# Kernel tuning notes

Measured on AMD Instinct MI355X. Metric: run time of the kernel, lower is better.

Reference implementation:

```python
import jax, jax.numpy as jnp
import numpy as np

B, S, HID = 1, 2048, 4096
H, HKV, D = 32, 8, 128
ROT = 64  # partial_rotary_factor = 0.5
EPS = 1e-6
SCALE = D ** -0.5


def setup_inputs() -> dict:
    key = jax.random.key(0)
    ks = jax.random.split(key, 8)
    return {
        "hidden_states": jax.random.normal(ks[0], (B, S, HID), jnp.float32),
        "cos": jax.random.uniform(ks[1], (B, S, ROT), jnp.float32),
        "sin": jax.random.uniform(ks[2], (B, S, ROT), jnp.float32),
        "Wq": jax.random.normal(ks[3], (H * D, HID), jnp.float32) * 0.02,
        "Wk": jax.random.normal(ks[4], (HKV * D, HID), jnp.float32) * 0.02,
        "Wv": jax.random.normal(ks[5], (HKV * D, HID), jnp.float32) * 0.02,
        "Wo": jax.random.normal(ks[6], (H * D, HID), jnp.float32).T * 0.02,  # [HID, H*D]
        "q_norm_w": jnp.ones((D,), jnp.float32),
        "k_norm_w": jnp.ones((D,), jnp.float32),
    }


def _rmsnorm(x, w):
    var = jnp.mean(jnp.square(x), axis=-1, keepdims=True)
    return x * jax.lax.rsqrt(var + EPS) * w


def _rotate_half(x):
    x1, x2 = jnp.split(x, 2, axis=-1)
    return jnp.concatenate([-x2, x1], axis=-1)


def reference(hidden_states, cos, sin, Wq, Wk, Wv, Wo, q_norm_w, k_norm_w):
    b, s, _ = hidden_states.shape
    q = (hidden_states @ Wq.T).reshape(b, s, H, D)
    k = (hidden_states @ Wk.T).reshape(b, s, HKV, D)
    v = (hidden_states @ Wv.T).reshape(b, s, HKV, D)
    # per-head QK RMSNorm
    q = _rmsnorm(q, q_norm_w)
    k = _rmsnorm(k, k_norm_w)
    # partial RoPE on first ROT dims; cos/sin broadcast over head dim (unsqueeze_dim=2)
    cs = cos[:, :, None, :]  # [B,S,1,ROT]
    sn = sin[:, :, None, :]
    q_rot, q_pass = q[..., :ROT], q[..., ROT:]
    k_rot, k_pass = k[..., :ROT], k[..., ROT:]
    q_rot = q_rot * cs + _rotate_half(q_rot) * sn
    k_rot = k_rot * cs + _rotate_half(k_rot) * sn
    q = jnp.concatenate([q_rot, q_pass], axis=-1)
    k = jnp.concatenate([k_rot, k_pass], axis=-1)
    # GQA: expand kv heads to query heads
    rep = H // HKV
    k = jnp.repeat(k, rep, axis=2)  # [B,S,H,D]
    v = jnp.repeat(v, rep, axis=2)
    # causal SDPA, bsnd layout
    scores = jnp.einsum("bqhd,bkhd->bhqk", q, k) * SCALE
    causal = jnp.tril(jnp.ones((s, s), bool))
    scores = jnp.where(causal, scores, jnp.finfo(scores.dtype).min)
    attn = jax.nn.softmax(scores, axis=-1)
    out = jnp.einsum("bhqk,bkhd->bqhd", attn, v).reshape(b, s, H * D)
    return out @ Wo.T
```

## Files before the change

### kernel.cpp

```cpp
#include <hip/hip_runtime.h>
#include <hip/hip_bf16.h>

typedef __attribute__((ext_vector_type(8))) short bf16x8;
typedef __attribute__((ext_vector_type(4))) float f32x4;
typedef __hip_bfloat16 bf16;

#define S_LEN 2048
#define HIDDEN 4096
#define NH 32
#define NKV 8
#define DH 128
#define ROTD 64
#define QKVW 6144
#define KOFF 4096
#define VOFF 5120
#define ATT_SCALE 0.08838834764831845f
#define RMS_EPS 1e-6f
#define KPITCH 136
#define VPITCH 72

#define BAR() __builtin_amdgcn_s_barrier()
#define VMCNT(n) asm volatile("s_waitcnt vmcnt(" #n ")" ::: "memory")
#define LGKM(n)  asm volatile("s_waitcnt lgkmcnt(" #n ")" ::: "memory")

static __device__ __forceinline__ unsigned short f2bu(float f) {
    bf16 h = __float2bfloat16(f);
    return __builtin_bit_cast(unsigned short, h);
}

static __device__ __forceinline__ void load_lds_16(const bf16* g, bf16* l) {
    __builtin_amdgcn_global_load_lds((const __attribute__((address_space(1))) void*)g,
                                     (__attribute__((address_space(3))) void*)l, 16, 0, 0);
}

__global__ __launch_bounds__(256) void cast_f32_bf16(const float* __restrict__ src,
                                                     unsigned short* __restrict__ dst, int n4) {
    int i = blockIdx.x * 256 + threadIdx.x;
    if (i >= n4) return;
    float4 v = reinterpret_cast<const float4*>(src)[i];
    ushort4 o;
    o.x = f2bu(v.x); o.y = f2bu(v.y); o.z = f2bu(v.z); o.w = f2bu(v.w);
    reinterpret_cast<ushort4*>(dst)[i] = o;
}

#define LDA_SUB(bufi, half) do {                                                        \
    const bf16* _ab = &As[bufi][half][0];                                               \
    _Pragma("unroll") for (int mf = 0; mf < 4; ++mf) {                                  \
        const int _r = arow + mf * 16;                                                  \
        _Pragma("unroll") for (int kk = 0; kk < 2; ++kk)                                \
            av[mf][kk] = *reinterpret_cast<const bf16x8*>(                              \
                _ab + (((_r << 6) + kk * 32 + quad * 8) ^ xorv));                       \
    } } while (0)

#define LDB_SUB(bufi, half, set) do {                                                   \
    const bf16* _bb = &Bs[bufi][half][0];                                               \
    _Pragma("unroll") for (int nf = 0; nf < 2; ++nf) {                                  \
        const int _r = brow + nf * 16;                                                  \
        _Pragma("unroll") for (int kk = 0; kk < 2; ++kk)                                \
            bv[set][nf][kk] = *reinterpret_cast<const bf16x8*>(                         \
                _bb + (((_r << 6) + kk * 32 + quad * 8) ^ xorv));                       \
    } } while (0)

#define MMQ(mh, nh, set) do {                                                           \
    _Pragma("unroll") for (int mf = 0; mf < 4; ++mf)                                    \
    _Pragma("unroll") for (int nf = 0; nf < 2; ++nf)                                    \
    _Pragma("unroll") for (int kk = 0; kk < 2; ++kk)                                    \
        acc[mh][nh][mf][nf] = __builtin_amdgcn_mfma_f32_16x16x32_bf16(                  \
            av[mf][kk], bv[set][nf][kk], acc[mh][nh][mf][nf], 0, 0, 0);                 \
    } while (0)

#define STAGE_A(bufi, half, tau) do {                                                   \
    const bf16* _s = Abase + (size_t)(half) * 128 * K + (size_t)(tau) * 64;             \
    load_lds_16(_s + sro0, &As[bufi][half][e0]);                                        \
    load_lds_16(_s + sro1, &As[bufi][half][e1]); } while (0)

#define STAGE_B(bufi, half, tau) do {                                                   \
    const bf16* _s = Bbase + (size_t)(half) * 128 * K + (size_t)(tau) * 64;             \
    load_lds_16(_s + sro0, &Bs[bufi][half][e0]);                                        \
    load_lds_16(_s + sro1, &Bs[bufi][half][e1]); } while (0)

template <typename OutT>
__global__ __launch_bounds__(512, 2) void gemm256(const bf16* __restrict__ A,
                                                  const bf16* __restrict__ B,
                                                  OutT* __restrict__ C,
                                                  int M, int N, int K) {
    __shared__ bf16 As[2][2][128 * 64];
    __shared__ bf16 Bs[2][2][128 * 64];

    const int tid  = threadIdx.x;
    const int lane = tid & 63;
    const int lq   = lane & 15;
    const int quad = lane >> 4;
    const int wave = tid >> 6;
    const int wr   = wave >> 2;
    const int wc   = wave & 3;

    const int nwg = gridDim.x;
    const int cpx = nwg >> 3;
    const int wg  = (blockIdx.x & 7) * cpx + (blockIdx.x >> 3);
    const int ntn = N >> 8;
    const int m0  = (wg / ntn) << 8;
    const int n0  = (wg % ntn) << 8;

    const int NT = K >> 6;

    const int d0 = tid * 16;
    const int d1 = 8192 + tid * 16;
    const int o0 = d0 ^ (((d0 >> 7) & 7) << 4);
    const int o1 = d1 ^ (((d1 >> 7) & 7) << 4);
    const int e0 = d0 >> 1;
    const int e1 = d1 >> 1;
    const size_t sro0 = (size_t)((o0 >> 1) >> 6) * K + ((o0 >> 1) & 63);
    const size_t sro1 = (size_t)((o1 >> 1) >> 6) * K + ((o1 >> 1) & 63);
    const bf16* Abase = A + (size_t)m0 * K;
    const bf16* Bbase = B + (size_t)n0 * K;

    const int arow = wr * 64 + lq;
    const int brow = wc * 32 + lq;
    const int xorv = (lq & 7) << 3;

    f32x4  acc[2][2][4][2] = {};
    bf16x8 av[4][2];
    bf16x8 bv[2][2][2];

    STAGE_B(0, 0, 0); STAGE_A(0, 0, 0); STAGE_B(0, 1, 0); STAGE_A(0, 1, 0);
    STAGE_B(1, 0, 1); STAGE_A(1, 0, 1); STAGE_B(1, 1, 1);
    VMCNT(6);
    BAR();

    for (int t = 0; t < NT; ++t) {
        const int buf = t & 1;

        LDA_SUB(buf, 0);
        LDB_SUB(buf, 0, 0);
        if (t + 1 < NT) STAGE_A(buf ^ 1, 1, t + 1);
        LGKM(8);
        BAR();
        LGKM(0);
        __builtin_amdgcn_s_setprio(1);
        MMQ(0, 0, 0);
        __builtin_amdgcn_s_setprio(0);
        BAR();

        LDB_SUB(buf, 1, 1);
        if (t + 2 < NT) STAGE_B(buf, 0, t + 2);
        BAR();
        LGKM(0);
        __builtin_amdgcn_s_setprio(1);
        MMQ(0, 1, 1);
        __builtin_amdgcn_s_setprio(0);
        BAR();

        LDA_SUB(buf, 1);
        if (t + 2 < NT) STAGE_A(buf, 0, t + 2);
        BAR();
        LGKM(0);
        __builtin_amdgcn_s_setprio(1);
        MMQ(1, 1, 1);
        __builtin_amdgcn_s_setprio(0);
        BAR();

        if (t + 2 < NT) STAGE_B(buf, 1, t + 2);
        BAR();
        __builtin_amdgcn_s_setprio(1);
        MMQ(1, 0, 0);
        __builtin_amdgcn_s_setprio(0);
        if (t < NT - 2) { VMCNT(6); } else { VMCNT(0); }
        BAR();
    }

#pragma unroll
    for (int mh = 0; mh < 2; ++mh)
#pragma unroll
        for (int nh = 0; nh < 2; ++nh)
#pragma unroll
            for (int mf = 0; mf < 4; ++mf)
#pragma unroll
                for (int nf = 0; nf < 2; ++nf)
#pragma unroll
                    for (int r = 0; r < 4; ++r) {
                        const int row = m0 + mh * 128 + wr * 64 + mf * 16 + quad * 4 + r;
                        const int col = n0 + nh * 128 + wc * 32 + nf * 16 + lq;
                        const float v = acc[mh][nh][mf][nf][r];
                        const size_t idx = (size_t)row * N + col;
                        if constexpr (sizeof(OutT) == 2) C[idx] = __float2bfloat16(v);
                        else                             C[idx] = v;
                    }
}

__global__ __launch_bounds__(256) void norm_rope(bf16* __restrict__ buf,
                                                 const float* __restrict__ w,
                                                 const float* __restrict__ cosp,
                                                 const float* __restrict__ sinp,
                                                 int log2nh, int stride, int coloff) {
    const int lane = threadIdx.x & 63;
    const int wave = threadIdx.x >> 6;
    const int row  = blockIdx.x * 4 + wave;
    const int s    = row >> log2nh;
    const int hh   = row & ((1 << log2nh) - 1);
    bf16* p = buf + (size_t)s * stride + coloff + hh * DH;

    float x1 = __bfloat162float(p[lane]);
    float x2 = __bfloat162float(p[64 + lane]);

    float ss = x1 * x1 + x2 * x2;
#pragma unroll
    for (int off = 1; off < 64; off <<= 1) ss += __shfl_xor(ss, off);
    float rs = rsqrtf(ss * (1.0f / 128.0f) + RMS_EPS);

    float y1 = x1 * rs * w[lane];
    float y2 = x2 * rs * w[64 + lane];

    float partner = __shfl_xor(y1, 32);
    float c  = cosp[(size_t)s * ROTD + lane];
    float sn = sinp[(size_t)s * ROTD + lane];
    float rot = (lane < 32) ? (y1 * c - partner * sn) : (y1 * c + partner * sn);

    p[lane]      = __float2bfloat16(rot);
    p[64 + lane] = __float2bfloat16(y2);
}

__global__ __launch_bounds__(256) void transpose_v(const bf16* __restrict__ v,
                                                   bf16* __restrict__ vt,
                                                   int stride, int colofs) {
    __shared__ bf16 t[32][65];
    const int c0 = blockIdx.x * 32;
    const int s0 = blockIdx.y * 64;
    {
        const int j  = threadIdx.x & 31;
        const int i0 = threadIdx.x >> 5;
#pragma unroll
        for (int p = 0; p < 8; ++p) {
            int si = p * 8 + i0;
            t[j][si] = v[(size_t)(s0 + si) * stride + colofs + c0 + j];
        }
    }
    __syncthreads();
    {
        const int ii = threadIdx.x & 63;
        const int j0 = threadIdx.x >> 6;
#pragma unroll
        for (int p = 0; p < 8; ++p) {
            int c = p * 4 + j0;
            vt[(size_t)(c0 + c) * S_LEN + s0 + ii] = t[c][ii];
        }
    }
}

struct FlashSmem {
    bf16 Ks[64][KPITCH];
    bf16 Vs[128][VPITCH];
    bf16 Ps[4][16][VPITCH];
};

static __device__ __forceinline__ void attn_qblock(int q0, int n_iter, int h, int kvh,
                                                   const bf16* __restrict__ QKV,
                                                   const bf16* __restrict__ VT,
                                                   bf16* __restrict__ O,
                                                   FlashSmem* sm) {
    const int tid  = threadIdx.x;
    const int lane = tid & 63;
    const int wave = tid >> 6;
    const int lq   = lane & 15;
    const int quad = lane >> 4;
    const int qr0  = q0 + wave * 16;

    bf16x8 qf[4];
    const bf16* qrow = QKV + (size_t)(qr0 + lq) * QKVW + h * DH + quad * 8;
#pragma unroll
    for (int i = 0; i < 4; ++i) {
        bf16x8 qv = *reinterpret_cast<const bf16x8*>(qrow + 32 * i);
#pragma unroll
        for (int j = 0; j < 8; ++j) {
            bf16 b = __builtin_bit_cast(bf16, (unsigned short)qv[j]);
            qv[j] = (short)__builtin_bit_cast(unsigned short,
                        __float2bfloat16(__bfloat162float(b) * ATT_SCALE));
        }
        qf[i] = qv;
    }

    f32x4 o[8];
#pragma unroll
    for (int t2 = 0; t2 < 8; ++t2) o[t2] = (f32x4){0.f, 0.f, 0.f, 0.f};
    float m_i[4], l_i[4];
#pragma unroll
    for (int r = 0; r < 4; ++r) { m_i[r] = -1e30f; l_i[r] = 0.f; }

    const bf16* kg = QKV + (size_t)(tid >> 2) * QKVW + KOFF + kvh * DH + (tid & 3) * 32;
    const bf16* vg = VT + (size_t)(kvh * DH + (tid >> 1)) * S_LEN + (tid & 1) * 32;
    bf16* ksl = &sm->Ks[tid >> 2][(tid & 3) * 32];
    bf16* vsl = &sm->Vs[tid >> 1][(tid & 1) * 32];
    bf16* pb  = &sm->Ps[wave][0][0];

    bf16x8 kreg[4], vreg[4];
#pragma unroll
    for (int c = 0; c < 4; ++c) {
        kreg[c] = *reinterpret_cast<const bf16x8*>(kg + 8 * c);
        vreg[c] = *reinterpret_cast<const bf16x8*>(vg + 8 * c);
    }

    for (int kt = 0; kt < n_iter; ++kt) {
        const int k0 = kt * 64;
#pragma unroll
        for (int c = 0; c < 4; ++c) {
            *reinterpret_cast<bf16x8*>(ksl + 8 * c) = kreg[c];
            *reinterpret_cast<bf16x8*>(vsl + 8 * c) = vreg[c];
        }
        __syncthreads();
        if (kt + 1 < n_iter) {
            const size_t kadv = (size_t)(kt + 1) * 64;
#pragma unroll
            for (int c = 0; c < 4; ++c) {
                kreg[c] = *reinterpret_cast<const bf16x8*>(kg + kadv * QKVW + 8 * c);
                vreg[c] = *reinterpret_cast<const bf16x8*>(vg + kadv + 8 * c);
            }
        }

        float p[4][4];
#pragma unroll
        for (int t = 0; t < 4; ++t) {
            f32x4 sacc = (f32x4){0.f, 0.f, 0.f, 0.f};
#pragma unroll
            for (int i = 0; i < 4; ++i) {
                bf16x8 kf = *reinterpret_cast<const bf16x8*>(&sm->Ks[t * 16 + lq][quad * 8 + 32 * i]);
                sacc = __builtin_amdgcn_mfma_f32_16x16x32_bf16(qf[i], kf, sacc, 0, 0, 0);
            }
#pragma unroll
            for (int r = 0; r < 4; ++r) {
                int qi = qr0 + quad * 4 + r;
                int ki = k0 + t * 16 + lq;
                p[t][r] = (ki > qi) ? -1e30f : sacc[r];
            }
        }

        float rowmax[4];
#pragma unroll
        for (int r = 0; r < 4; ++r)
            rowmax[r] = fmaxf(fmaxf(p[0][r], p[1][r]), fmaxf(p[2][r], p[3][r]));
#pragma unroll
        for (int off = 1; off < 16; off <<= 1)
#pragma unroll
            for (int r = 0; r < 4; ++r) rowmax[r] = fmaxf(rowmax[r], __shfl_xor(rowmax[r], off));

        float alpha[4];
#pragma unroll
        for (int r = 0; r < 4; ++r) {
            float mn = fmaxf(m_i[r], rowmax[r]);
            alpha[r] = __expf(m_i[r] - mn);
            m_i[r] = mn;
        }
#pragma unroll
        for (int t = 0; t < 4; ++t)
#pragma unroll
            for (int r = 0; r < 4; ++r) p[t][r] = __expf(p[t][r] - m_i[r]);

        float rsum[4];
#pragma unroll
        for (int r = 0; r < 4; ++r) rsum[r] = (p[0][r] + p[1][r]) + (p[2][r] + p[3][r]);
#pragma unroll
        for (int off = 1; off < 16; off <<= 1)
#pragma unroll
            for (int r = 0; r < 4; ++r) rsum[r] += __shfl_xor(rsum[r], off);
#pragma unroll
        for (int r = 0; r < 4; ++r) l_i[r] = l_i[r] * alpha[r] + rsum[r];

#pragma unroll
        for (int t = 0; t < 4; ++t)
#pragma unroll
            for (int r = 0; r < 4; ++r)
                pb[(quad * 4 + r) * VPITCH + t * 16 + lq] = __float2bfloat16(p[t][r]);
        __threadfence_block();

#pragma unroll
        for (int t2 = 0; t2 < 8; ++t2)
#pragma unroll
            for (int r = 0; r < 4; ++r) o[t2][r] *= alpha[r];

#pragma unroll
        for (int hh = 0; hh < 2; ++hh) {
            bf16x8 pa = *reinterpret_cast<const bf16x8*>(pb + lq * VPITCH + hh * 32 + quad * 8);
#pragma unroll
            for (int t2 = 0; t2 < 8; ++t2) {
                bf16x8 vf = *reinterpret_cast<const bf16x8*>(&sm->Vs[t2 * 16 + lq][hh * 32 + quad * 8]);
                o[t2] = __builtin_amdgcn_mfma_f32_16x16x32_bf16(pa, vf, o[t2], 0, 0, 0);
            }
        }
        __syncthreads();
    }

#pragma unroll
    for (int r = 0; r < 4; ++r) l_i[r] = 1.0f / l_i[r];
#pragma unroll
    for (int t2 = 0; t2 < 8; ++t2)
#pragma unroll
        for (int r = 0; r < 4; ++r)
            O[(size_t)(qr0 + quad * 4 + r) * (NH * DH) + h * DH + t2 * 16 + lq] =
                __float2bfloat16(o[t2][r] * l_i[r]);
}

__global__ __launch_bounds__(256) void flash_attn(const bf16* __restrict__ QKV,
                                                  const bf16* __restrict__ VT,
                                                  bf16* __restrict__ O) {
    __shared__ FlashSmem sm;
    const int b  = blockIdx.x;
    const int h  = b & 31;
    const int pr = b >> 5;
    const int kvh = h >> 2;
    attn_qblock((31 - pr) * 64, 32 - pr, h, kvh, QKV, VT, O, &sm);
    __syncthreads();
    attn_qblock(pr * 64,        pr + 1,  h, kvh, QKV, VT, O, &sm);
}

extern "C" void kernel_launch(void* const* d_in, const int* in_sizes, int n_in,
                              void* d_out, int out_size, void* d_ws, size_t ws_size,
                              hipStream_t stream) {
    const float* hs   = (const float*)d_in[0];
    const float* cosp = (const float*)d_in[1];
    const float* sinp = (const float*)d_in[2];
    const float* Wq   = (const float*)d_in[3];
    const float* Wk   = (const float*)d_in[4];
    const float* Wv   = (const float*)d_in[5];
    const float* Wo   = (const float*)d_in[6];
    const float* qw   = (const float*)d_in[7];
    const float* kw   = (const float*)d_in[8];
    float* out = (float*)d_out;

    char* ws = (char*)d_ws;
    size_t off = 0;
    auto carve = [&](size_t bytes) { char* p = ws + off; off += (bytes + 255) & ~(size_t)255; return p; };

    bf16* hsb  = (bf16*)carve((size_t)S_LEN * HIDDEN * 2);
    bf16* wqkv = (bf16*)carve((size_t)QKVW * HIDDEN * 2);
    bf16* wob  = (bf16*)carve((size_t)HIDDEN * NH * DH * 2);
    bf16* qkv  = (bf16*)carve((size_t)S_LEN * QKVW * 2);
    bf16* vtb  = (bf16*)carve((size_t)NKV * DH * S_LEN * 2);

    cast_f32_bf16<<<(S_LEN * HIDDEN / 4 + 255) / 256, 256, 0, stream>>>(hs, (unsigned short*)hsb, S_LEN * HIDDEN / 4);
    cast_f32_bf16<<<(NH * DH * HIDDEN / 4 + 255) / 256, 256, 0, stream>>>(Wq, (unsigned short*)wqkv, NH * DH * HIDDEN / 4);
    cast_f32_bf16<<<(NKV * DH * HIDDEN / 4 + 255) / 256, 256, 0, stream>>>(Wk, (unsigned short*)(wqkv + (size_t)KOFF * HIDDEN), NKV * DH * HIDDEN / 4);
    cast_f32_bf16<<<(NKV * DH * HIDDEN / 4 + 255) / 256, 256, 0, stream>>>(Wv, (unsigned short*)(wqkv + (size_t)VOFF * HIDDEN), NKV * DH * HIDDEN / 4);
    cast_f32_bf16<<<(HIDDEN * NH * DH / 4 + 255) / 256, 256, 0, stream>>>(Wo, (unsigned short*)wob, HIDDEN * NH * DH / 4);

    gemm256<bf16><<<dim3((S_LEN / 256) * (QKVW / 256)), 512, 0, stream>>>(hsb, wqkv, qkv, S_LEN, QKVW, HIDDEN);

    norm_rope<<<S_LEN * NH / 4, 256, 0, stream>>>(qkv, qw, cosp, sinp, 5, QKVW, 0);
    norm_rope<<<S_LEN * NKV / 4, 256, 0, stream>>>(qkv, kw, cosp, sinp, 3, QKVW, KOFF);

    transpose_v<<<dim3(NKV * DH / 32, S_LEN / 64), 256, 0, stream>>>(qkv, vtb, QKVW, VOFF);

    bf16* aob = hsb;
    flash_attn<<<512, 256, 0, stream>>>(qkv, vtb, aob);

    gemm256<float><<<dim3((S_LEN / 256) * (HIDDEN / 256)), 512, 0, stream>>>(aob, wob, out, S_LEN, HIDDEN, NH * DH);
}
```

Baseline: 563.0 us.

## Fuse casts, swizzle QKV GEMM tiles, split attention blocks, smaller Wo GEMM

Merges the five fp32-to-bf16 cast launches into one kernel, which saves launch overhead. The QKV GEMM gets a 2D XCD-aware tile swizzle so each XCD reuses a shared block of A rows and B columns. Flash attention now launches one query block per workgroup (1024 blocks) instead of pairing a long and a short block. The output projection moves to a simpler 128x128 GEMM without double buffering, which adds parallelism but may lose pipelining efficiency.

```diff
diff --git a/kernel.cpp b/kernel.cpp
--- a/kernel.cpp
+++ b/kernel.cpp
@@ -33,14 +33,25 @@
                                      (__attribute__((address_space(3))) void*)l, 16, 0, 0);
 }
 
-__global__ __launch_bounds__(256) void cast_f32_bf16(const float* __restrict__ src,
-                                                     unsigned short* __restrict__ dst, int n4) {
-    int i = blockIdx.x * 256 + threadIdx.x;
-    if (i >= n4) return;
-    float4 v = reinterpret_cast<const float4*>(src)[i];
+__global__ __launch_bounds__(256) void cast_all(const float* __restrict__ hs,
+                                                const float* __restrict__ Wq,
+                                                const float* __restrict__ Wk,
+                                                const float* __restrict__ Wv,
+                                                const float* __restrict__ Wo,
+                                                unsigned short* __restrict__ hsb,
+                                                unsigned short* __restrict__ wqkv,
+                                                unsigned short* __restrict__ wob) {
+    const int i = blockIdx.x * 256 + threadIdx.x;
+    const float* src; unsigned short* dst; int j;
+    if (i < 2097152)      { src = hs; dst = hsb;  j = i; }
+    else if (i < 6291456) { src = Wq; dst = wqkv; j = i - 2097152; }
+    else if (i < 7340032) { src = Wk; dst = wqkv + (size_t)KOFF * HIDDEN; j = i - 6291456; }
+    else if (i < 8388608) { src = Wv; dst = wqkv + (size_t)VOFF * HIDDEN; j = i - 7340032; }
+    else                  { src = Wo; dst = wob;  j = i - 8388608; }
+    float4 v = reinterpret_cast<const float4*>(src)[j];
     ushort4 o;
     o.x = f2bu(v.x); o.y = f2bu(v.y); o.z = f2bu(v.z); o.w = f2bu(v.w);
-    reinterpret_cast<ushort4*>(dst)[i] = o;
+    reinterpret_cast<ushort4*>(dst)[j] = o;
 }
 
 #define LDA_SUB(bufi, half) do {                                                        \
@@ -83,7 +94,8 @@
 __global__ __launch_bounds__(512, 2) void gemm256(const bf16* __restrict__ A,
                                                   const bf16* __restrict__ B,
                                                   OutT* __restrict__ C,
-                                                  int M, int N, int K) {
+                                                  int M, int N, int K, int ktiles,
+                                                  int swz2d) {
     __shared__ bf16 As[2][2][128 * 64];
     __shared__ bf16 Bs[2][2][128 * 64];
 
@@ -95,14 +107,24 @@
     const int wr   = wave >> 2;
     const int wc   = wave & 3;
 
-    const int nwg = gridDim.x;
-    const int cpx = nwg >> 3;
-    const int wg  = (blockIdx.x & 7) * cpx + (blockIdx.x >> 3);
-    const int ntn = N >> 8;
-    const int m0  = (wg / ntn) << 8;
-    const int n0  = (wg % ntn) << 8;
-
-    const int NT = K >> 6;
+    int m0, n0;
+    if (swz2d) {
+        const int xcd = blockIdx.x & 7;
+        const int loc = blockIdx.x >> 3;
+        const int lm  = loc / 6;
+        const int ln  = loc - lm * 6;
+        m0 = (((xcd >> 2) << 2) + lm) << 8;
+        n0 = ((xcd & 3) * 6 + ln) << 8;
+    } else {
+        const int nwg = gridDim.x;
+        const int cpx = nwg >> 3;
+        const int wg  = (blockIdx.x & 7) * cpx + (blockIdx.x >> 3);
+        const int ntn = N >> 8;
+        m0 = (wg / ntn) << 8;
+        n0 = (wg % ntn) << 8;
+    }
+
+    const int NT = ktiles;
 
     const int d0 = tid * 16;
     const int d1 = 8192 + tid * 16;
@@ -186,6 +208,70 @@
                         if constexpr (sizeof(OutT) == 2) C[idx] = __float2bfloat16(v);
                         else                             C[idx] = v;
                     }
+}
+
+template <typename OutT>
+__global__ __launch_bounds__(256) void gemm_lds(const bf16* __restrict__ A,
+                                                const bf16* __restrict__ B,
+                                                OutT* __restrict__ C,
+                                                int M, int N, int K) {
+    __shared__ bf16 As[128 * 32];
+    __shared__ bf16 Bs[128 * 32];
+    const int tid  = threadIdx.x;
+    const int lane = tid & 63;
+    const int wave = tid >> 6;
+    const int lq   = lane & 15;
+    const int quad = lane >> 4;
+    const int m0 = blockIdx.y * 128;
+    const int n0 = blockIdx.x * 128;
+    const int wm = (wave & 1) * 64;
+    const int wn = (wave >> 1) * 64;
+
+    f32x4 acc[4][4] = {};
+
+    const int ar = tid >> 2;
+    const int ac = (tid & 3) * 8;
+    const bf16* Ag0 = A + (size_t)(m0 + ar) * K + ac;
+    const bf16* Ag1 = Ag0 + (size_t)64 * K;
+    const bf16* Bg0 = B + (size_t)(n0 + ar) * K + ac;
+    const bf16* Bg1 = Bg0 + (size_t)64 * K;
+    bf16* Asl0 = As + wave * 512;
+    bf16* Asl1 = As + wave * 512 + 2048;
+    bf16* Bsl0 = Bs + wave * 512;
+    bf16* Bsl1 = Bs + wave * 512 + 2048;
+
+    for (int k0 = 0; k0 < K; k0 += 32) {
+        load_lds_16(Ag0 + k0, Asl0);
+        load_lds_16(Ag1 + k0, Asl1);
+        load_lds_16(Bg0 + k0, Bsl0);
+        load_lds_16(Bg1 + k0, Bsl1);
+        __syncthreads();
+        bf16x8 avv[4], bvv[4];
+#pragma unroll
+        for (int i = 0; i < 4; ++i)
+            avv[i] = *reinterpret_cast<const bf16x8*>(As + (wm + i * 16 + lq) * 32 + quad * 8);
+#pragma unroll
+        for (int i = 0; i < 4; ++i)
+            bvv[i] = *reinterpret_cast<const bf16x8*>(Bs + (wn + i * 16 + lq) * 32 + quad * 8);
+#pragma unroll
+        for (int mt = 0; mt < 4; ++mt)
+#pragma unroll
+            for (int nt = 0; nt < 4; ++nt)
+                acc[mt][nt] = __builtin_amdgcn_mfma_f32_16x16x32_bf16(avv[mt], bvv[nt], acc[mt][nt], 0, 0, 0);
+        __syncthreads();
+    }
+
+#pragma unroll
+    for (int mt = 0; mt < 4; ++mt)
+#pragma unroll
+        for (int nt = 0; nt < 4; ++nt)
+#pragma unroll
+            for (int r = 0; r < 4; ++r) {
+                float v = acc[mt][nt][r];
+                size_t idx = (size_t)(m0 + wm + mt * 16 + quad * 4 + r) * N + n0 + wn + nt * 16 + lq;
+                if constexpr (sizeof(OutT) == 2) C[idx] = __float2bfloat16(v);
+                else                             C[idx] = v;
+            }
 }
 
 __global__ __launch_bounds__(256) void norm_rope(bf16* __restrict__ buf,
@@ -404,11 +490,9 @@
     __shared__ FlashSmem sm;
     const int b  = blockIdx.x;
     const int h  = b & 31;
-    const int pr = b >> 5;
+    const int qb = 31 - (b >> 5);
     const int kvh = h >> 2;
-    attn_qblock((31 - pr) * 64, 32 - pr, h, kvh, QKV, VT, O, &sm);
-    __syncthreads();
-    attn_qblock(pr * 64,        pr + 1,  h, kvh, QKV, VT, O, &sm);
+    attn_qblock(qb * 64, qb + 1, h, kvh, QKV, VT, O, &sm);
 }
 
 extern "C" void kernel_launch(void* const* d_in, const int* in_sizes, int n_in,
@@ -435,13 +519,12 @@
     bf16* qkv  = (bf16*)carve((size_t)S_LEN * QKVW * 2);
     bf16* vtb  = (bf16*)carve((size_t)NKV * DH * S_LEN * 2);
 
-    cast_f32_bf16<<<(S_LEN * HIDDEN / 4 + 255) / 256, 256, 0, stream>>>(hs, (unsigned short*)hsb, S_LEN * HIDDEN / 4);
-    cast_f32_bf16<<<(NH * DH * HIDDEN / 4 + 255) / 256, 256, 0, stream>>>(Wq, (unsigned short*)wqkv, NH * DH * HIDDEN / 4);
-    cast_f32_bf16<<<(NKV * DH * HIDDEN / 4 + 255) / 256, 256, 0, stream>>>(Wk, (unsigned short*)(wqkv + (size_t)KOFF * HIDDEN), NKV * DH * HIDDEN / 4);
-    cast_f32_bf16<<<(NKV * DH * HIDDEN / 4 + 255) / 256, 256, 0, stream>>>(Wv, (unsigned short*)(wqkv + (size_t)VOFF * HIDDEN), NKV * DH * HIDDEN / 4);
-    cast_f32_bf16<<<(HIDDEN * NH * DH / 4 + 255) / 256, 256, 0, stream>>>(Wo, (unsigned short*)wob, HIDDEN * NH * DH / 4);
-
-    gemm256<bf16><<<dim3((S_LEN / 256) * (QKVW / 256)), 512, 0, stream>>>(hsb, wqkv, qkv, S_LEN, QKVW, HIDDEN);
+    cast_all<<<49152, 256, 0, stream>>>(hs, Wq, Wk, Wv, Wo,
+                                        (unsigned short*)hsb, (unsigned short*)wqkv,
+                                        (unsigned short*)wob);
+
+    gemm256<bf16><<<dim3(192), 512, 0, stream>>>(
+        hsb, wqkv, qkv, S_LEN, QKVW, HIDDEN, HIDDEN / 64, 1);
 
     norm_rope<<<S_LEN * NH / 4, 256, 0, stream>>>(qkv, qw, cosp, sinp, 5, QKVW, 0);
     norm_rope<<<S_LEN * NKV / 4, 256, 0, stream>>>(qkv, kw, cosp, sinp, 3, QKVW, KOFF);
@@ -449,7 +532,8 @@
     transpose_v<<<dim3(NKV * DH / 32, S_LEN / 64), 256, 0, stream>>>(qkv, vtb, QKVW, VOFF);
 
     bf16* aob = hsb;
-    flash_attn<<<512, 256, 0, stream>>>(qkv, vtb, aob);
-
-    gemm256<float><<<dim3((S_LEN / 256) * (HIDDEN / 256)), 512, 0, stream>>>(aob, wob, out, S_LEN, HIDDEN, NH * DH);
-}
+    flash_attn<<<1024, 256, 0, stream>>>(qkv, vtb, aob);
+
+    gemm_lds<float><<<dim3(HIDDEN / 128, S_LEN / 128), 256, 0, stream>>>(
+        aob, wob, out, S_LEN, HIDDEN, NH * DH);
+}
```

Result: faster. 539.9 us (-4.1%).
